# Kernel optimization log

Hardware: AMD Instinct MI355X
Metric: run time of the kernel (lower is better)

## Reference

```python
import jax, jax.numpy as jnp
import numpy as np

STAGE_SHAPES = {
    'stage1': [(12, 10, 3, 3), (12, 12, 3, 3), (12, 12, 3, 3)],
    'stage2': [(24, 22, 3, 3), (24, 24, 3, 3), (12, 24, 3, 3)],
    'stage3': [(24, 22, 3, 3), (24, 24, 3, 3), (12, 24, 3, 3)],
    'stage4': [(11, 22, 1, 1)],
}
BN_CH = [12, 12, 12, 24, 24, 12, 24, 24, 12]  # channels of the 9 BN layers, in forward order
OFF = np.concatenate([[0], np.cumsum(BN_CH)]).tolist()
EPS = 1e-5


def _split_weights(wflat, shapes):
    """Slice flat [B, P] hypernet weights into per-layer [B, O, I, k, k] tensors."""
    outs, bg = [], 0
    for s in shapes:
        n = int(np.prod(s))
        outs.append(wflat[:, bg:bg + n].reshape((-1,) + s))
        bg += n
    return outs


def _per_sample_conv(x, w):
    """x: [B, C, H, W], w: [B, O, C, k, k] -> [B, O, H, W]. Each sample uses its own filters (SAME padding = k//2 for odd k)."""
    def one(xi, wi):
        return jax.lax.conv_general_dilated(
            xi[None], wi, window_strides=(1, 1), padding='SAME',
            dimension_numbers=('NCHW', 'OIHW', 'NCHW'))[0]
    return jax.vmap(one)(x, w)


def _bn_eval(y, gamma, beta, mean, var):
    """Eval-mode BatchNorm2d over channel dim of [B, C, H, W]."""
    inv = gamma * jax.lax.rsqrt(var + EPS)
    return y * inv[None, :, None, None] + (beta - mean * inv)[None, :, None, None]


def setup_inputs():
    key = jax.random.key(0)
    ks = jax.random.split(key, 8)
    B, H, W = 64, 128, 128
    x = jax.random.normal(ks[0], (B, 10, H, W), jnp.float32)
    # scale hypernet weights down so 9 stacked convs stay numerically tame
    w_stage1 = jax.random.normal(ks[1], (B, 3672), jnp.float32) * 0.05
    w_stage2 = jax.random.normal(ks[2], (B, 12528), jnp.float32) * 0.05
    w_stage3 = jax.random.normal(ks[3], (B, 12528), jnp.float32) * 0.05
    w_stage4 = jax.random.normal(ks[4], (B, 242), jnp.float32) * 0.05
    n_bn = sum(BN_CH)  # 144
    bn_gamma = jax.random.uniform(ks[5], (n_bn,), jnp.float32, 0.5, 1.5)
    bn_beta = jax.random.normal(ks[6], (n_bn,), jnp.float32) * 0.1
    bn_mean = jnp.zeros((n_bn,), jnp.float32)
    bn_var = jnp.ones((n_bn,), jnp.float32)
    return dict(x=x, w_stage1=w_stage1, w_stage2=w_stage2, w_stage3=w_stage3,
                w_stage4=w_stage4, bn_gamma=bn_gamma, bn_beta=bn_beta,
                bn_mean=bn_mean, bn_var=bn_var)


def reference(x, w_stage1, w_stage2, w_stage3, w_stage4, bn_gamma, bn_beta, bn_mean, bn_var):
    cur = x
    li = 0  # global BN layer index
    for stage_key, wflat in (('stage1', w_stage1), ('stage2', w_stage2), ('stage3', w_stage3)):
        for w in _split_weights(wflat, STAGE_SHAPES[stage_key]):
            conv = _per_sample_conv(cur, w)
            lo, hi = OFF[li], OFF[li + 1]
            bn = _bn_eval(conv, bn_gamma[lo:hi], bn_beta[lo:hi], bn_mean[lo:hi], bn_var[lo:hi])
            cur = jax.nn.relu(bn)
            li += 1
        cur = jnp.concatenate([cur, x], axis=1)  # dense skip: [B, 12+10, H, W]
    w_pred = _split_weights(w_stage4, STAGE_SHAPES['stage4'])[0]  # [B, 11, 22, 1, 1]
    return _per_sample_conv(cur, w_pred)
```

## Files before the change

### kernel.cpp

```cpp
#include <hip/hip_runtime.h>
#include <stdint.h>

#define HW    16384
#define NB    64
#define W2    130
#define PXS   (W2*W2)
#define WQH   70144
#define EPSB  1e-5f
#define PXB   48
#define PROWB (38*PXB)
#define PLH   34656

typedef _Float16 h8  __attribute__((ext_vector_type(8)));
typedef _Float16 h4  __attribute__((ext_vector_type(4)));
typedef float    f16v __attribute__((ext_vector_type(16)));
typedef float    f4  __attribute__((ext_vector_type(4)));
typedef h8 uh8 __attribute__((aligned(4)));
typedef h4 uh4 __attribute__((aligned(4)));
typedef f4 uf4 __attribute__((aligned(4)));

__global__ void prep_w(const float* __restrict__ w1, const float* __restrict__ w2,
                       const float* __restrict__ w3, const float* __restrict__ w4,
                       const float* __restrict__ g,  const float* __restrict__ be,
                       const float* __restrict__ mu, const float* __restrict__ va,
                       _Float16* __restrict__ wq, float* __restrict__ bias)
{
    const int FO[11]   = {0,576,1152,1728,2880,4032,5184,6336,7488,8640,8768};
    const int start[10]= {0,1080,2376,3672,8424,13608,16200,20952,26136,28728};
    const int COt[10]  = {12,12,12,24,24,12,24,24,12,11};
    const int CIt[10]  = {10,12,12,22,24,24,22,24,24,22};
    const int bnoff[10]= {0,12,24,36,60,84,96,120,144,0};
    const int KST[10]  = {1,1,1,2,2,2,2,2,2,2};

    long tid = (long)blockIdx.x * 256 + threadIdx.x;
    long total = (long)NB * 8768, stride = (long)gridDim.x * 256;
    for (long idx = tid; idx < total; idx += stride) {
        int b = (int)(idx / 8768), i = (int)(idx - (long)b * 8768);
        int l = 9; while (i < FO[l]) --l;
        int j = i - FO[l];
        int f = j >> 6, lane = j & 63;
        int ks = (KST[l] == 2) ? (f & 1) : 0;
        int s  = (KST[l] == 2) ? (f >> 1) : f;
        int co = lane & 31, hi = lane >> 5;
        int CO = COt[l], CI = CIt[l];
        float scale = 1.f;
        if (l < 9 && co < CO) {
            int bi = bnoff[l] + co;
            scale = g[bi] * rsqrtf(va[bi] + EPSB);
        }
        int c0 = ks * 16 + hi * 8;
        __attribute__((aligned(16))) _Float16 vals[8];
#pragma unroll
        for (int e = 0; e < 8; ++e) {
            int c = c0 + e; float wv = 0.f;
            if (co < CO && c < CI) {
                int p = (l < 9) ? start[l] + (co * CI + c) * 9 + s
                                : start[9] + co * CI + c;
                const float* src; long si;
                if      (p <  3672) { src = w1; si = (long)b *  3672 + p; }
                else if (p < 16200) { src = w2; si = (long)b * 12528 + (p -  3672); }
                else if (p < 28728) { src = w3; si = (long)b * 12528 + (p - 16200); }
                else                { src = w4; si = (long)b *   242 + (p - 28728); }
                wv = src[si] * scale;
            }
            vals[e] = (_Float16)wv;
        }
        *(uh8*)(wq + idx * 8) = *(const h8*)vals;
    }
    if (tid < 320) {
        int l = (int)tid >> 5, co = (int)tid & 31;
        float v = 0.f;
        if (l < 9 && co < COt[l]) {
            int bi = bnoff[l] + co;
            float sc = g[bi] * rsqrtf(va[bi] + EPSB);
            v = be[bi] - mu[bi] * sc;
        }
        bias[tid] = v;
    }
}

__global__ void pad_x(const float* __restrict__ x, _Float16* __restrict__ bufA,
                      _Float16* __restrict__ bufB, int b0)
{
    int sl = blockIdx.x >> 3, part = blockIdx.x & 7;
    int gb = b0 + sl;
    const float* __restrict__ xs = x + (long)gb * 10 * HW;
    _Float16* __restrict__ dA = bufA + (long)sl * PXS * 32;
    _Float16* __restrict__ dB = bufB + (long)sl * PXS * 32;
    for (int p = part * 256 + threadIdx.x; p < PXS; p += 2048) {
        int r = p / W2, cc = p - r * W2;
        __attribute__((aligned(16))) _Float16 pxA[32], pxB[32];
#pragma unroll
        for (int i = 0; i < 32; ++i) { pxA[i] = (_Float16)0.f; pxB[i] = (_Float16)0.f; }
        if (r >= 1 && r <= 128 && cc >= 1 && cc <= 128) {
            int so = (r - 1) * 128 + (cc - 1);
#pragma unroll
            for (int c = 0; c < 10; ++c) {
                _Float16 xv = (_Float16)xs[c * HW + so];
                pxA[c] = xv; pxA[12 + c] = xv; pxB[12 + c] = xv;
            }
        }
        _Float16* ap = dA + (long)p * 32;
        _Float16* bp = dB + (long)p * 32;
#pragma unroll
        for (int q = 0; q < 4; ++q) {
            *(uh8*)(ap + q * 8) = *(const h8*)(pxA + q * 8);
            *(uh8*)(bp + q * 8) = *(const h8*)(pxB + q * 8);
        }
    }
}

template<int KST>
__device__ __forceinline__ void lconv(const char* pin, char* pout,
    const _Float16* wl, const float* __restrict__ bias, int boff,
    int rowStart, int nRows, int colStart, int width,
    int oy0, int ox0, int w, int lo5, int hi)
{
    constexpr int FR = 9 * KST;
    h8 afr[FR];
#pragma unroll
    for (int f = 0; f < FR; ++f) afr[f] = *(const uh8*)(wl + (long)f * 512);
    f4 bv[4];
#pragma unroll
    for (int q = 0; q < 4; ++q) bv[q] = *(const uf4*)(bias + boff + hi * 4 + q * 8);
    constexpr int qmax = (KST == 1) ? 2 : 3;

    const int ncb = (width > 32) ? 2 : 1;
    const int nrg = (nRows + 3) >> 2;
    const int nu  = nrg * ncb;
#pragma unroll 1
    for (int u = w; u < nu; u += 4) {
        int rg, cb;
        if (ncb == 2) { rg = u >> 1; cb = u & 1; } else { rg = u; cb = 0; }
        const int r0   = rowStart + rg * 4;
        const int cs   = cb ? (colStart + width - 32) : colStart;
        const int cmin = cb ? (64 - width) : 0;
        const char* bin = pin + (long)(cs - 1 + lo5) * PXB + hi * 16;

        f16v acc[4];
        { f16v z = {}; acc[0] = z; acc[1] = z; acc[2] = z; acc[3] = z; }

#pragma unroll
        for (int kc = 0; kc < 3; ++kc)
#pragma unroll
        for (int ks = 0; ks < KST; ++ks) {
            h8 bf[6];
#pragma unroll
            for (int j = 0; j < 6; ++j) {
                int rr = r0 - 1 + j; rr = (rr > 37) ? 37 : rr;
                h8 v = {};
                if (!(ks & hi))
                    v = *(const uh8*)(bin + (long)rr * PROWB + kc * PXB + ks * 32);
                bf[j] = v;
            }
#pragma unroll
            for (int kr = 0; kr < 3; ++kr) {
                h8 af = afr[(kr * 3 + kc) * KST + ks];
#pragma unroll
                for (int tt = 0; tt < 4; ++tt)
                    acc[tt] = __builtin_amdgcn_mfma_f32_32x32x16_f16(af, bf[kr + tt], acc[tt], 0, 0, 0);
            }
        }

        const bool cok = (lo5 >= cmin);
        const int  pc  = cs + lo5;
        const int  gx  = ox0 - 3 + pc;
        const bool xin = (unsigned)(gx - 1) < 128u;
#pragma unroll
        for (int tt = 0; tt < 4; ++tt) {
            int pr = r0 + tt;
            if (pr >= rowStart + nRows) continue;
            int gy = oy0 - 3 + pr;
            bool ok = xin && ((unsigned)(gy - 1) < 128u);
            char* po = pout + ((long)pr * 38 + pc) * PXB + hi * 8;
            if (cok) {
#pragma unroll
                for (int q = 0; q < qmax; ++q) {
                    float v0 = ok ? fmaxf(acc[tt][4*q+0] + bv[q][0], 0.f) : 0.f;
                    float v1 = ok ? fmaxf(acc[tt][4*q+1] + bv[q][1], 0.f) : 0.f;
                    float v2 = ok ? fmaxf(acc[tt][4*q+2] + bv[q][2], 0.f) : 0.f;
                    float v3 = ok ? fmaxf(acc[tt][4*q+3] + bv[q][3], 0.f) : 0.f;
                    h4 hv = { (_Float16)v0, (_Float16)v1, (_Float16)v2, (_Float16)v3 };
                    *(uh4*)(po + q * 16) = hv;
                }
            }
        }
    }
}

template<int KST>
__global__ __launch_bounds__(256, 1)
void stage3(const _Float16* __restrict__ in, _Float16* __restrict__ out,
            const _Float16* __restrict__ wq, int loff0,
            const float* __restrict__ bias, int boff0, int b0)
{
    __shared__ _Float16 lds[2][PLH];
    const int t = threadIdx.x, w = t >> 6, l = t & 63;
    const int lo5 = l & 31, hi = l >> 5;

    const int nbb = (int)(gridDim.x >> 4);
    int s, tile;
    if ((nbb & 7) == 0) {
        int xcd = (int)(blockIdx.x & 7), j = (int)(blockIdx.x >> 3);
        s = xcd * (nbb >> 3) + (j >> 4); tile = j & 15;
    } else { s = (int)(blockIdx.x >> 4); tile = (int)(blockIdx.x & 15); }
    const int gb  = b0 + s;
    const int oy0 = 1 + (tile >> 2) * 32;
    const int ox0 = 1 + (tile & 3) * 32;

    {
        const char* src = (const char*)(in + (long)s * PXS * 32);
        char* dst = (char*)&lds[0][0];
        h8 stg[17];
#pragma unroll
        for (int k = 0; k < 17; ++k) {
            int idx = k * 256 + t;
            int r = idx / 114, g2 = idx - r * 114;
            int p = g2 / 3,   c  = g2 - p * 3;
            int gy = oy0 - 3 + r, gx = ox0 - 3 + p;
            h8 v = {};
            if (idx < 4332 && (unsigned)gy < 130u && (unsigned)gx < 130u)
                v = *(const uh8*)(src + ((long)gy * W2 + gx) * 64 + c * 16);
            stg[k] = v;
        }
#pragma unroll
        for (int k = 0; k < 17; ++k) {
            int idx = k * 256 + t;
            if (idx < 4332) *(uh8*)(dst + (long)idx * 16) = stg[k];
        }
    }
    __syncthreads();

    const _Float16* wl = wq + (long)gb * WQH + loff0 + (long)l * 8;
    constexpr int LSTEP = 9 * KST * 512;
    lconv<KST>((const char*)lds[0], (char*)lds[1], wl,             bias, boff0,      1, 36, 1, 36, oy0, ox0, w, lo5, hi);
    __syncthreads();
    lconv<KST>((const char*)lds[1], (char*)lds[0], wl + LSTEP,     bias, boff0 + 32, 2, 34, 2, 34, oy0, ox0, w, lo5, hi);
    __syncthreads();
    lconv<KST>((const char*)lds[0], (char*)lds[1], wl + 2 * LSTEP, bias, boff0 + 64, 3, 32, 3, 32, oy0, ox0, w, lo5, hi);
    __syncthreads();

    {
        _Float16* db = out + (long)s * PXS * 32;
        const char* T = (const char*)&lds[1][0];
#pragma unroll
        for (int k = 0; k < 4; ++k) {
            int px = k * 256 + t;
            int pr = 3 + (px >> 5), pc = 3 + (px & 31);
            int gy = oy0 + (px >> 5), gx = ox0 + (px & 31);
            const char* sp = T + ((long)pr * 38 + pc) * PXB;
            h8 v0 = *(const uh8*)sp;
            h4 v1 = *(const uh4*)(sp + 16);
            _Float16* dp = db + ((long)gy * W2 + gx) * 32;
            *(uh8*)dp = v0;
            *(uh4*)(dp + 8) = v1;
        }
    }
}

__global__ __launch_bounds__(256, 2)
void conv1(const _Float16* __restrict__ in, float* __restrict__ outF,
           const _Float16* __restrict__ wq, int loff, int b0)
{
    const int s = blockIdx.y, gb = b0 + s;
    const int t = threadIdx.x, w = t >> 6, l = t & 63;
    const int lo5 = l & 31, hi = l >> 5;
    const int cb = blockIdx.x & 3;
    const int y00 = (blockIdx.x >> 2) * 32 + w * 8;
    const int xpix = cb * 32 + lo5;

    const _Float16* wl = wq + (long)gb * WQH + loff + (long)l * 8;
    h8 a0 = *(const uh8*)(wl);
    h8 a1 = *(const uh8*)(wl + 512);
    const _Float16* ib = in + (long)s * PXS * 32;

#pragma unroll 1
    for (int tt = 0; tt < 8; ++tt) {
        int y = y00 + tt;
        const _Float16* bp = ib + ((long)(y + 1) * W2 + xpix + 1) * 32 + hi * 8;
        h8 bA = *(const uh8*)(bp);
        h8 bB = *(const uh8*)(bp + 16);
        f16v acc = {};
        acc = __builtin_amdgcn_mfma_f32_32x32x16_f16(a0, bA, acc, 0, 0, 0);
        acc = __builtin_amdgcn_mfma_f32_32x32x16_f16(a1, bB, acc, 0, 0, 0);
        long px = (long)y * 128 + xpix;
#pragma unroll
        for (int r = 0; r < 16; ++r) {
            int co = (r & 3) + 8 * (r >> 2) + 4 * hi;
            if (co < 11) outF[((long)gb * 11 + co) * HW + px] = acc[r];
        }
    }
}

extern "C" void kernel_launch(void* const* d_in, const int* in_sizes, int n_in,
                              void* d_out, int out_size, void* d_ws, size_t ws_size,
                              hipStream_t stream)
{
    const float *x = (const float*)d_in[0], *w1 = (const float*)d_in[1],
                *w2 = (const float*)d_in[2], *w3 = (const float*)d_in[3],
                *w4 = (const float*)d_in[4], *g  = (const float*)d_in[5],
                *be = (const float*)d_in[6], *mu = (const float*)d_in[7],
                *va = (const float*)d_in[8];
    if (n_in == 9) {
        const float* big801[2] = {nullptr, nullptr}; int n801 = 0;
        const float* bn156[4]  = {nullptr, nullptr, nullptr, nullptr}; int n156 = 0;
        const float *fx = nullptr, *fw1 = nullptr, *fw4 = nullptr;
        for (int i = 0; i < 9; ++i) {
            int sz = in_sizes[i];
            if      (sz == 10485760) fx  = (const float*)d_in[i];
            else if (sz ==   235008) fw1 = (const float*)d_in[i];
            else if (sz ==   801792) { if (n801 < 2) big801[n801++] = (const float*)d_in[i]; }
            else if (sz ==    15488) fw4 = (const float*)d_in[i];
            else if (sz ==      156) { if (n156 < 4) bn156[n156++] = (const float*)d_in[i]; }
        }
        if (fx && fw1 && fw4 && n801 == 2 && n156 == 4) {
            x = fx; w1 = fw1; w2 = big801[0]; w3 = big801[1]; w4 = fw4;
            g = bn156[0]; be = bn156[1]; mu = bn156[2]; va = bn156[3];
        }
    }
    float* out = (float*)d_out;

    const size_t wqB   = (size_t)NB * WQH * 2;
    const size_t biasB = 2048;
    const size_t hdr   = wqB + biasB;
    const size_t perSlot = (size_t)PXS * 128;
    size_t avail = ws_size > hdr ? ws_size - hdr : 0;
    int chunk = (int)(avail / perSlot);
    if (chunk > NB) chunk = NB;
    if (chunk < 1)  chunk = 1;

    _Float16* wq   = (_Float16*)d_ws;
    float*    bias = (float*)((char*)d_ws + wqB);
    _Float16* bufA = (_Float16*)((char*)d_ws + hdr);
    _Float16* bufB = bufA + (size_t)chunk * PXS * 32;

    prep_w<<<2048, 256, 0, stream>>>(w1, w2, w3, w4, g, be, mu, va, wq, bias);

    for (int b0 = 0; b0 < NB; b0 += chunk) {
        int nb = (NB - b0 < chunk) ? (NB - b0) : chunk;
        pad_x<<<nb * 8, 256, 0, stream>>>(x, bufA, bufB, b0);
        int gc = nb * 16;
        dim3 g1(16, nb);
        stage3<1><<<gc, 256, 0, stream>>>(bufA, bufB, wq,     0, bias,   0, b0);
        stage3<2><<<gc, 256, 0, stream>>>(bufB, bufA, wq, 13824, bias,  96, b0);
        stage3<2><<<gc, 256, 0, stream>>>(bufA, bufB, wq, 41472, bias, 192, b0);
        conv1<<<g1, 256, 0, stream>>>(bufB, out, wq, 69120, b0);
    }
}
```

Measured before the change: 537.8 us.

## Use 12 waves per stage block with smaller row groups and streamed weights

Raises the fused stage kernel from 4 to 12 wavefronts per block so each block's three convolution layers are spread over more waves. Row groups shrink to 3 rows for the first two layers and stay at 4 for the last. Weight fragments are now loaded inside the inner loop instead of being kept in registers, which lowers register pressure so the larger block fits. The costs are repeated weight loads from global memory or cache, less reuse of each B fragment per MFMA, and possible load imbalance when the row-group count does not divide evenly across 12 waves.

```diff
diff --git a/kernel.cpp b/kernel.cpp
--- a/kernel.cpp
+++ b/kernel.cpp
@@ -10,6 +10,8 @@
 #define PXB   48
 #define PROWB (38*PXB)
 #define PLH   34656
+#define NTH   768
+#define NWV   12
 
 typedef _Float16 h8  __attribute__((ext_vector_type(8)));
 typedef _Float16 h4  __attribute__((ext_vector_type(4)));
@@ -110,43 +112,41 @@
     }
 }
 
-template<int KST>
+template<int KST, int NR>
 __device__ __forceinline__ void lconv(const char* pin, char* pout,
     const _Float16* wl, const float* __restrict__ bias, int boff,
     int rowStart, int nRows, int colStart, int width,
     int oy0, int ox0, int w, int lo5, int hi)
 {
-    constexpr int FR = 9 * KST;
-    h8 afr[FR];
-#pragma unroll
-    for (int f = 0; f < FR; ++f) afr[f] = *(const uh8*)(wl + (long)f * 512);
     f4 bv[4];
 #pragma unroll
     for (int q = 0; q < 4; ++q) bv[q] = *(const uf4*)(bias + boff + hi * 4 + q * 8);
     constexpr int qmax = (KST == 1) ? 2 : 3;
 
     const int ncb = (width > 32) ? 2 : 1;
-    const int nrg = (nRows + 3) >> 2;
+    const int nrg = (nRows + NR - 1) / NR;
     const int nu  = nrg * ncb;
 #pragma unroll 1
-    for (int u = w; u < nu; u += 4) {
+    for (int u = w; u < nu; u += NWV) {
         int rg, cb;
         if (ncb == 2) { rg = u >> 1; cb = u & 1; } else { rg = u; cb = 0; }
-        const int r0   = rowStart + rg * 4;
+        const int r0   = rowStart + rg * NR;
         const int cs   = cb ? (colStart + width - 32) : colStart;
         const int cmin = cb ? (64 - width) : 0;
         const char* bin = pin + (long)(cs - 1 + lo5) * PXB + hi * 16;
 
-        f16v acc[4];
-        { f16v z = {}; acc[0] = z; acc[1] = z; acc[2] = z; acc[3] = z; }
+        f16v acc[NR];
+        { f16v z = {};
+#pragma unroll
+          for (int i = 0; i < NR; ++i) acc[i] = z; }
 
 #pragma unroll
         for (int kc = 0; kc < 3; ++kc)
 #pragma unroll
         for (int ks = 0; ks < KST; ++ks) {
-            h8 bf[6];
-#pragma unroll
-            for (int j = 0; j < 6; ++j) {
+            h8 bf[NR + 2];
+#pragma unroll
+            for (int j = 0; j < NR + 2; ++j) {
                 int rr = r0 - 1 + j; rr = (rr > 37) ? 37 : rr;
                 h8 v = {};
                 if (!(ks & hi))
@@ -155,9 +155,9 @@
             }
 #pragma unroll
             for (int kr = 0; kr < 3; ++kr) {
-                h8 af = afr[(kr * 3 + kc) * KST + ks];
-#pragma unroll
-                for (int tt = 0; tt < 4; ++tt)
+                h8 af = *(const uh8*)(wl + ((kr * 3 + kc) * KST + ks) * 512);
+#pragma unroll
+                for (int tt = 0; tt < NR; ++tt)
                     acc[tt] = __builtin_amdgcn_mfma_f32_32x32x16_f16(af, bf[kr + tt], acc[tt], 0, 0, 0);
             }
         }
@@ -167,7 +167,7 @@
         const int  gx  = ox0 - 3 + pc;
         const bool xin = (unsigned)(gx - 1) < 128u;
 #pragma unroll
-        for (int tt = 0; tt < 4; ++tt) {
+        for (int tt = 0; tt < NR; ++tt) {
             int pr = r0 + tt;
             if (pr >= rowStart + nRows) continue;
             int gy = oy0 - 3 + pr;
@@ -189,7 +189,7 @@
 }
 
 template<int KST>
-__global__ __launch_bounds__(256, 1)
+__global__ __launch_bounds__(NTH)
 void stage3(const _Float16* __restrict__ in, _Float16* __restrict__ out,
             const _Float16* __restrict__ wq, int loff0,
             const float* __restrict__ bias, int boff0, int b0)
@@ -211,10 +211,10 @@
     {
         const char* src = (const char*)(in + (long)s * PXS * 32);
         char* dst = (char*)&lds[0][0];
-        h8 stg[17];
-#pragma unroll
-        for (int k = 0; k < 17; ++k) {
-            int idx = k * 256 + t;
+        h8 stg[6];
+#pragma unroll
+        for (int k = 0; k < 6; ++k) {
+            int idx = k * NTH + t;
             int r = idx / 114, g2 = idx - r * 114;
             int p = g2 / 3,   c  = g2 - p * 3;
             int gy = oy0 - 3 + r, gx = ox0 - 3 + p;
@@ -224,8 +224,8 @@
             stg[k] = v;
         }
 #pragma unroll
-        for (int k = 0; k < 17; ++k) {
-            int idx = k * 256 + t;
+        for (int k = 0; k < 6; ++k) {
+            int idx = k * NTH + t;
             if (idx < 4332) *(uh8*)(dst + (long)idx * 16) = stg[k];
         }
     }
@@ -233,27 +233,29 @@
 
     const _Float16* wl = wq + (long)gb * WQH + loff0 + (long)l * 8;
     constexpr int LSTEP = 9 * KST * 512;
-    lconv<KST>((const char*)lds[0], (char*)lds[1], wl,             bias, boff0,      1, 36, 1, 36, oy0, ox0, w, lo5, hi);
+    lconv<KST,3>((const char*)lds[0], (char*)lds[1], wl,             bias, boff0,      1, 36, 1, 36, oy0, ox0, w, lo5, hi);
     __syncthreads();
-    lconv<KST>((const char*)lds[1], (char*)lds[0], wl + LSTEP,     bias, boff0 + 32, 2, 34, 2, 34, oy0, ox0, w, lo5, hi);
+    lconv<KST,3>((const char*)lds[1], (char*)lds[0], wl + LSTEP,     bias, boff0 + 32, 2, 34, 2, 34, oy0, ox0, w, lo5, hi);
     __syncthreads();
-    lconv<KST>((const char*)lds[0], (char*)lds[1], wl + 2 * LSTEP, bias, boff0 + 64, 3, 32, 3, 32, oy0, ox0, w, lo5, hi);
+    lconv<KST,4>((const char*)lds[0], (char*)lds[1], wl + 2 * LSTEP, bias, boff0 + 64, 3, 32, 3, 32, oy0, ox0, w, lo5, hi);
     __syncthreads();
 
     {
         _Float16* db = out + (long)s * PXS * 32;
         const char* T = (const char*)&lds[1][0];
 #pragma unroll
-        for (int k = 0; k < 4; ++k) {
-            int px = k * 256 + t;
-            int pr = 3 + (px >> 5), pc = 3 + (px & 31);
-            int gy = oy0 + (px >> 5), gx = ox0 + (px & 31);
-            const char* sp = T + ((long)pr * 38 + pc) * PXB;
-            h8 v0 = *(const uh8*)sp;
-            h4 v1 = *(const uh4*)(sp + 16);
-            _Float16* dp = db + ((long)gy * W2 + gx) * 32;
-            *(uh8*)dp = v0;
-            *(uh4*)(dp + 8) = v1;
+        for (int k = 0; k < 2; ++k) {
+            int px = k * NTH + t;
+            if (px < 1024) {
+                int pr = 3 + (px >> 5), pc = 3 + (px & 31);
+                int gy = oy0 + (px >> 5), gx = ox0 + (px & 31);
+                const char* sp = T + ((long)pr * 38 + pc) * PXB;
+                h8 v0 = *(const uh8*)sp;
+                h4 v1 = *(const uh4*)(sp + 16);
+                _Float16* dp = db + ((long)gy * W2 + gx) * 32;
+                *(uh8*)dp = v0;
+                *(uh4*)(dp + 8) = v1;
+            }
         }
     }
 }
@@ -341,9 +343,9 @@
         pad_x<<<nb * 8, 256, 0, stream>>>(x, bufA, bufB, b0);
         int gc = nb * 16;
         dim3 g1(16, nb);
-        stage3<1><<<gc, 256, 0, stream>>>(bufA, bufB, wq,     0, bias,   0, b0);
-        stage3<2><<<gc, 256, 0, stream>>>(bufB, bufA, wq, 13824, bias,  96, b0);
-        stage3<2><<<gc, 256, 0, stream>>>(bufA, bufB, wq, 41472, bias, 192, b0);
+        stage3<1><<<gc, NTH, 0, stream>>>(bufA, bufB, wq,     0, bias,   0, b0);
+        stage3<2><<<gc, NTH, 0, stream>>>(bufB, bufA, wq, 13824, bias,  96, b0);
+        stage3<2><<<gc, NTH, 0, stream>>>(bufA, bufB, wq, 41472, bias, 192, b0);
         conv1<<<g1, 256, 0, stream>>>(bufB, out, wq, 69120, b0);
     }
 }
```

After: 475.9 us. 1.13x faster.
